# Kernel optimization log

Measured on AMD Instinct MI355X. Metric: run time of the kernel, lower is better.

Reference implementation:

```python
import jax, jax.numpy as jnp
import numpy as np

B, N, K = 8, 128, 8
N_HEADS, LATENT = 8, 128
D = N_HEADS * LATENT  # total_dim = 1024


def setup_inputs() -> dict:
    key = jax.random.key(0)
    ks = jax.random.split(key, 9)
    embedded = jax.random.normal(ks[0], (B, N, D), dtype=jnp.float32)
    # CoLight-style one-hot neighbor-selection adjacency: [B, N, K, N]
    nbr_idx = jax.random.randint(ks[1], (B, N, K), 0, N)
    adj_matrix = jax.nn.one_hot(nbr_idx, N, dtype=jnp.float32)
    s = 1.0 / np.sqrt(D)
    Wl = jax.random.uniform(ks[2], (D, D), jnp.float32, -s, s)
    bl = jax.random.uniform(ks[3], (D,), jnp.float32, -s, s)
    Wa = jax.random.uniform(ks[4], (D, D), jnp.float32, -s, s)
    ba = jax.random.uniform(ks[5], (D,), jnp.float32, -s, s)
    Wh = jax.random.uniform(ks[6], (D, D), jnp.float32, -s, s)
    bh = jax.random.uniform(ks[7], (D,), jnp.float32, -s, s)
    return {"embedded": embedded, "adj_matrix": adj_matrix,
            "Wl": Wl, "bl": bl, "Wa": Wa, "ba": ba, "Wh": Wh, "bh": bh}


def reference(embedded, adj_matrix, Wl, bl, Wa, ba, Wh, bh):
    b, n, d = embedded.shape
    H, L = N_HEADS, LATENT
    # torch: tile embedded to [B,N,N,D] then matmul with adj [B,N,K,N].
    # Equivalent without materializing the tile:
    neighbor_embed = jnp.einsum('bikn,bnd->bikd', adj_matrix, embedded)  # [B,N,K,D]

    agent = jax.nn.relu(embedded @ Wl + bl)                      # [B,N,D]
    # reshape (B,N,1,L,H) then permute (0,1,4,2,3) -> [B,N,H,1,L]
    agent_heads = agent.reshape(b, n, 1, L, H).transpose(0, 1, 4, 2, 3)

    nb = jax.nn.relu(neighbor_embed @ Wa + ba)
    neighbor_heads = nb.reshape(b, n, -1, L, H).transpose(0, 1, 4, 2, 3)  # [B,N,H,K,L]

    # einsum 'ijklm,ijknm->ijklm' with l=1: agent * sum over neighbors
    attn = agent_heads * neighbor_heads.sum(axis=3, keepdims=True)  # [B,N,H,1,L]
    attn = jax.nn.softmax(attn, axis=-1)

    nh = jax.nn.relu(neighbor_embed @ Wh + bh)
    neighbor_hidden = nh.reshape(b, n, -1, L, H).transpose(0, 1, 4, 2, 3)  # [B,N,H,K,L]

    out = attn * neighbor_hidden.sum(axis=3, keepdims=True)  # [B,N,H,1,L]
    out = out.mean(axis=2)                                   # [B,N,1,L]
    return out.reshape(b, n, -1)                             # [B,N,L]
```

## Files before the change

### kernel.cpp

```cpp
#include <hip/hip_runtime.h>
#include <math.h>

#define DD 1024
#define NN 128
#define BB 8
#define KNBR 8
#define NH 8
#define LL 128

typedef __attribute__((ext_vector_type(8))) short short8v;
typedef __attribute__((ext_vector_type(4))) float f32x4;

#define GLDS(gptr, lptr)                                                      \
  __builtin_amdgcn_global_load_lds(                                           \
      (const __attribute__((address_space(1))) void*)(gptr),                  \
      (__attribute__((address_space(3))) void*)(lptr), 16, 0, 0)

__device__ __forceinline__ unsigned short f2bf(float x) {
  unsigned u = __float_as_uint(x);
  unsigned r = u + 0x7fff + ((u >> 16) & 1);
  return (unsigned short)(r >> 16);
}
__device__ __forceinline__ float bf2f(unsigned short u) {
  return __uint_as_float((unsigned)u << 16);
}

__global__ __launch_bounds__(256)
void prep(const float* __restrict__ E,
          const float* __restrict__ Wl, const float* __restrict__ Wa,
          const float* __restrict__ Wh,
          unsigned short* __restrict__ Eb, unsigned short* __restrict__ Wt) {
  const int z = blockIdx.z;
  const int t = threadIdx.x;

  if (z == 3) {
    const int bid = blockIdx.y * 16 + blockIdx.x;
    const int i0 = bid * 4096 + t * 16;
    #pragma unroll
    for (int q = 0; q < 2; ++q) {
      const int i = i0 + q * 8;
      float4 a = *(const float4*)&E[i];
      float4 c = *(const float4*)&E[i + 4];
      union { unsigned short u[8]; uint4 v; } o;
      o.u[0] = f2bf(a.x); o.u[1] = f2bf(a.y); o.u[2] = f2bf(a.z); o.u[3] = f2bf(a.w);
      o.u[4] = f2bf(c.x); o.u[5] = f2bf(c.y); o.u[6] = f2bf(c.z); o.u[7] = f2bf(c.w);
      *(uint4*)&Eb[i] = o.v;
    }
    return;
  }

  const float* W = (z == 0) ? Wl : (z == 1) ? Wa : Wh;
  unsigned short* out = Wt + (size_t)z * DD * DD;

  __shared__ unsigned short tile[64][65];
  const int tx = t & 15, ty = t >> 4;
  const int r0 = blockIdx.y * 64, c0 = blockIdx.x * 64;

  #pragma unroll
  for (int i = 0; i < 4; ++i) {
    const int r = ty + i * 16;
    float4 v = *(const float4*)&W[(size_t)(r0 + r) * DD + c0 + tx * 4];
    tile[r][tx * 4 + 0] = f2bf(v.x);
    tile[r][tx * 4 + 1] = f2bf(v.y);
    tile[r][tx * 4 + 2] = f2bf(v.z);
    tile[r][tx * 4 + 3] = f2bf(v.w);
  }
  __syncthreads();
  #pragma unroll
  for (int i = 0; i < 4; ++i) {
    const int rr = ty + i * 16;
    ushort4 o;
    o.x = tile[tx * 4 + 0][rr];
    o.y = tile[tx * 4 + 1][rr];
    o.z = tile[tx * 4 + 2][rr];
    o.w = tile[tx * 4 + 3][rr];
    *(ushort4*)&out[(size_t)(c0 + rr) * DD + r0 + tx * 4] = o;
  }
}

__global__ __launch_bounds__(256)
void gemm3_mfma(const unsigned short* __restrict__ Eb,
                const unsigned short* __restrict__ Wt,
                const float* __restrict__ bl, const float* __restrict__ ba,
                const float* __restrict__ bh,
                float* __restrict__ Yl, unsigned short* __restrict__ Yab,
                unsigned short* __restrict__ Yhb) {
  const int orig = blockIdx.x;
  const int job = (orig & 7) * 96 + (orig >> 3);
  const int mat = job >> 8;
  const int rem = job & 255;
  const int bx = rem >> 4;
  const int by = rem & 15;

  const unsigned short* Bg = Wt + (size_t)mat * DD * DD;
  const float* bias = (mat == 0) ? bl : (mat == 1) ? ba : bh;

  __shared__ unsigned short As[3][64 * 64];
  __shared__ unsigned short Bs[3][64 * 64];

  const int t = threadIdx.x;
  const int lane = t & 63;
  const int w = t >> 6;
  const int wr = w >> 1, wc = w & 1;
  const int brow = by * 64, bcol = bx * 64;

  const int srow = t >> 3;
  const int sk = (((t & 7) ^ (srow & 7)) * 8);
  const unsigned short* gA = Eb + (size_t)(brow + srow) * DD + sk;
  const unsigned short* gB = Bg + (size_t)(bcol + srow) * DD + sk;
  const int ldsoff = w * 512;

  const int lrow = lane & 15, lg = lane >> 4;

  int aidx[2][2], bidx[2][2];
  #pragma unroll
  for (int kk = 0; kk < 2; ++kk)
    #pragma unroll
    for (int m = 0; m < 2; ++m) {
      const int ra = wr * 32 + m * 16 + lrow;
      aidx[kk][m] = ra * 64 + (((kk * 4 + lg) ^ (ra & 7)) * 8);
      const int rb = wc * 32 + m * 16 + lrow;
      bidx[kk][m] = rb * 64 + (((kk * 4 + lg) ^ (rb & 7)) * 8);
    }

  float bv0 = bias[bcol + wc * 32 + lrow];
  float bv1 = bias[bcol + wc * 32 + 16 + lrow];
  asm volatile("" : "+v"(bv0), "+v"(bv1));

  f32x4 acc[2][2] = {};

#define STAGE(q, kt) do {                                                     \
    const int k0_ = (kt) * 64;                                                \
    GLDS(gA + k0_,           &As[q][ldsoff]);                                 \
    GLDS(gA + k0_ + 32 * DD, &As[q][2048 + ldsoff]);                          \
    GLDS(gB + k0_,           &Bs[q][ldsoff]);                                 \
    GLDS(gB + k0_ + 32 * DD, &Bs[q][2048 + ldsoff]);                          \
  } while (0)

  STAGE(0, 0);
  STAGE(1, 1);

  #pragma unroll
  for (int kt = 0; kt < 16; ++kt) {
    const int p = kt % 3;
    if (kt != 15) asm volatile("s_waitcnt vmcnt(4)" ::: "memory");
    else          asm volatile("s_waitcnt vmcnt(0)" ::: "memory");
    __builtin_amdgcn_s_barrier();
    if (kt + 2 < 16) STAGE((kt + 2) % 3, kt + 2);

    short8v a[2][2], b[2][2];
    #pragma unroll
    for (int kk = 0; kk < 2; ++kk)
      #pragma unroll
      for (int m = 0; m < 2; ++m) {
        a[kk][m] = *(const short8v*)&As[p][aidx[kk][m]];
        b[kk][m] = *(const short8v*)&Bs[p][bidx[kk][m]];
      }

    #pragma unroll
    for (int kk = 0; kk < 2; ++kk)
      #pragma unroll
      for (int m = 0; m < 2; ++m)
        #pragma unroll
        for (int n = 0; n < 2; ++n)
          acc[m][n] = __builtin_amdgcn_mfma_f32_16x16x32_bf16(
              a[kk][m], b[kk][n], acc[m][n], 0, 0, 0);
  }
#undef STAGE

  #pragma unroll
  for (int m = 0; m < 2; ++m) {
    #pragma unroll
    for (int n = 0; n < 2; ++n) {
      const int col = bcol + wc * 32 + n * 16 + lrow;
      const int r0  = brow + wr * 32 + m * 16 + lg * 4;
      const float bv = n ? bv1 : bv0;
      if (mat == 0) {
        #pragma unroll
        for (int j = 0; j < 4; ++j)
          Yl[(size_t)(r0 + j) * DD + col] = fmaxf(acc[m][n][j] + bv, 0.f);
      } else {
        unsigned short* Yo = (mat == 1) ? Yab : Yhb;
        #pragma unroll
        for (int j = 0; j < 4; ++j)
          Yo[(size_t)(r0 + j) * DD + col] = f2bf(fmaxf(acc[m][n][j] + bv, 0.f));
      }
    }
  }
}

__global__ __launch_bounds__(256)
void colight_epilogue(const float* __restrict__ adj,
                      const float* __restrict__ Yl,
                      const unsigned short* __restrict__ Yab,
                      const unsigned short* __restrict__ Yhb,
                      float* __restrict__ out) {
  const int bid = blockIdx.x;
  const int bi = (bid & 7) * NN + (bid >> 3);
  const int b  = bi >> 7;

  __shared__ int   idxs[KNBR];
  __shared__ float sA[DD];
  __shared__ float sH[DD];
  __shared__ float sL[DD];
  __shared__ float sPart[NH][LL];

  const int t = threadIdx.x;

  const float* arow = adj + (size_t)bi * KNBR * NN;
  {
    const int k = t >> 5, j = t & 31;
    float4 v = *(const float4*)&arow[k * NN + j * 4];
    const int base = j * 4;
    if (v.x > 0.5f) idxs[k] = base;
    if (v.y > 0.5f) idxs[k] = base + 1;
    if (v.z > 0.5f) idxs[k] = base + 2;
    if (v.w > 0.5f) idxs[k] = base + 3;
  }
  __syncthreads();

  const int rbase = b * NN;
  int ridx[KNBR];
  #pragma unroll
  for (int k = 0; k < KNBR; ++k) ridx[k] = rbase + idxs[k];

  const int d0 = t * 4;
  {
    float a0 = 0.f, a1 = 0.f, a2 = 0.f, a3 = 0.f;
    float h0 = 0.f, h1 = 0.f, h2 = 0.f, h3 = 0.f;
    #pragma unroll
    for (int k = 0; k < KNBR; ++k) {
      const size_t rr = (size_t)ridx[k] * DD + d0;
      ushort4 va = *(const ushort4*)&Yab[rr];
      ushort4 vh = *(const ushort4*)&Yhb[rr];
      a0 += bf2f(va.x); a1 += bf2f(va.y); a2 += bf2f(va.z); a3 += bf2f(va.w);
      h0 += bf2f(vh.x); h1 += bf2f(vh.y); h2 += bf2f(vh.z); h3 += bf2f(vh.w);
    }
    float4 sa = {a0, a1, a2, a3};
    float4 sh = {h0, h1, h2, h3};
    *(float4*)&sA[d0] = sa;
    *(float4*)&sH[d0] = sh;
    *(float4*)&sL[d0] = *(const float4*)&Yl[(size_t)bi * DD + d0];
  }
  __syncthreads();

  const int h = t >> 5, j = t & 31;
  float z[4];
  float mx = -1e30f;
  #pragma unroll
  for (int q = 0; q < 4; ++q) {
    const int l = j + q * 32;
    z[q] = sL[l * NH + h] * sA[l * NH + h];
    mx = fmaxf(mx, z[q]);
  }
  #pragma unroll
  for (int m = 1; m <= 16; m <<= 1)
    mx = fmaxf(mx, __shfl_xor(mx, m, 32));

  float se = 0.f;
  #pragma unroll
  for (int q = 0; q < 4; ++q) {
    z[q] = expf(z[q] - mx);
    se += z[q];
  }
  #pragma unroll
  for (int m = 1; m <= 16; m <<= 1)
    se += __shfl_xor(se, m, 32);
  const float inv = 1.f / se;

  #pragma unroll
  for (int q = 0; q < 4; ++q) {
    const int l = j + q * 32;
    sPart[h][l] = z[q] * inv * sH[l * NH + h] * 0.125f;
  }
  __syncthreads();

  if (t < LL) {
    float o = 0.f;
    #pragma unroll
    for (int hh = 0; hh < NH; ++hh) o += sPart[hh][t];
    out[(size_t)bi * LL + t] = o;
  }
}

extern "C" void kernel_launch(void* const* d_in, const int* in_sizes, int n_in,
                              void* d_out, int out_size, void* d_ws, size_t ws_size,
                              hipStream_t stream) {
  const float* E   = (const float*)d_in[0];
  const float* adj = (const float*)d_in[1];
  const float* Wl  = (const float*)d_in[2];
  const float* bl  = (const float*)d_in[3];
  const float* Wa  = (const float*)d_in[4];
  const float* ba  = (const float*)d_in[5];
  const float* Wh  = (const float*)d_in[6];
  const float* bh  = (const float*)d_in[7];
  float* out = (float*)d_out;

  char* ws = (char*)d_ws;
  float*          Yl  = (float*)ws;
  unsigned short* Yab = (unsigned short*)(ws + 4  * 1024 * 1024);
  unsigned short* Yhb = (unsigned short*)(ws + 6  * 1024 * 1024);
  unsigned short* Eb  = (unsigned short*)(ws + 8  * 1024 * 1024);
  unsigned short* Wt  = (unsigned short*)(ws + 10 * 1024 * 1024);

  prep<<<dim3(16, 16, 4), dim3(256), 0, stream>>>(E, Wl, Wa, Wh, Eb, Wt);
  gemm3_mfma<<<dim3(768), dim3(256), 0, stream>>>(Eb, Wt, bl, ba, bh,
                                                  Yl, Yab, Yhb);
  colight_epilogue<<<dim3(BB * NN), dim3(256), 0, stream>>>(adj, Yl, Yab, Yhb, out);
}
```

Baseline: 28.89 us.

## Store agent projection in bf16, transpose epilogue LDS layout, add MFMA priority

The fp32 agent-projection output becomes bf16, so all three GEMM outputs share one store path and the epilogue reads half the bytes for that tensor. The epilogue's shared arrays are re-laid out as [head][latent], which removes the strided l*NH+h accesses that caused bank conflicts. It also wraps the MFMA loop in s_setprio and switches expf to __expf. The cost is lost precision in the agent projection and in the exponential.

```diff
diff --git a/kernel.cpp b/kernel.cpp
--- a/kernel.cpp
+++ b/kernel.cpp
@@ -83,7 +83,8 @@
                 const unsigned short* __restrict__ Wt,
                 const float* __restrict__ bl, const float* __restrict__ ba,
                 const float* __restrict__ bh,
-                float* __restrict__ Yl, unsigned short* __restrict__ Yab,
+                unsigned short* __restrict__ Ylb,
+                unsigned short* __restrict__ Yab,
                 unsigned short* __restrict__ Yhb) {
   const int orig = blockIdx.x;
   const int job = (orig & 7) * 96 + (orig >> 3);
@@ -157,6 +158,7 @@
         b[kk][m] = *(const short8v*)&Bs[p][bidx[kk][m]];
       }
 
+    __builtin_amdgcn_s_setprio(1);
     #pragma unroll
     for (int kk = 0; kk < 2; ++kk)
       #pragma unroll
@@ -165,9 +167,11 @@
         for (int n = 0; n < 2; ++n)
           acc[m][n] = __builtin_amdgcn_mfma_f32_16x16x32_bf16(
               a[kk][m], b[kk][n], acc[m][n], 0, 0, 0);
+    __builtin_amdgcn_s_setprio(0);
   }
 #undef STAGE
 
+  unsigned short* Yo = (mat == 0) ? Ylb : (mat == 1) ? Yab : Yhb;
   #pragma unroll
   for (int m = 0; m < 2; ++m) {
     #pragma unroll
@@ -175,23 +179,16 @@
       const int col = bcol + wc * 32 + n * 16 + lrow;
       const int r0  = brow + wr * 32 + m * 16 + lg * 4;
       const float bv = n ? bv1 : bv0;
-      if (mat == 0) {
-        #pragma unroll
-        for (int j = 0; j < 4; ++j)
-          Yl[(size_t)(r0 + j) * DD + col] = fmaxf(acc[m][n][j] + bv, 0.f);
-      } else {
-        unsigned short* Yo = (mat == 1) ? Yab : Yhb;
-        #pragma unroll
-        for (int j = 0; j < 4; ++j)
-          Yo[(size_t)(r0 + j) * DD + col] = f2bf(fmaxf(acc[m][n][j] + bv, 0.f));
-      }
+      #pragma unroll
+      for (int j = 0; j < 4; ++j)
+        Yo[(size_t)(r0 + j) * DD + col] = f2bf(fmaxf(acc[m][n][j] + bv, 0.f));
     }
   }
 }
 
 __global__ __launch_bounds__(256)
 void colight_epilogue(const float* __restrict__ adj,
-                      const float* __restrict__ Yl,
+                      const unsigned short* __restrict__ Ylb,
                       const unsigned short* __restrict__ Yab,
                       const unsigned short* __restrict__ Yhb,
                       float* __restrict__ out) {
@@ -200,9 +197,9 @@
   const int b  = bi >> 7;
 
   __shared__ int   idxs[KNBR];
-  __shared__ float sA[DD];
-  __shared__ float sH[DD];
-  __shared__ float sL[DD];
+  __shared__ float sA[NH][LL];
+  __shared__ float sH[NH][LL];
+  __shared__ float sL[NH][LL];
   __shared__ float sPart[NH][LL];
 
   const int t = threadIdx.x;
@@ -225,22 +222,26 @@
   for (int k = 0; k < KNBR; ++k) ridx[k] = rbase + idxs[k];
 
   const int d0 = t * 4;
+  const int gl = t >> 1;
+  const int h0 = (t & 1) * 4;
   {
     float a0 = 0.f, a1 = 0.f, a2 = 0.f, a3 = 0.f;
-    float h0 = 0.f, h1 = 0.f, h2 = 0.f, h3 = 0.f;
+    float g0 = 0.f, g1 = 0.f, g2 = 0.f, g3 = 0.f;
     #pragma unroll
     for (int k = 0; k < KNBR; ++k) {
       const size_t rr = (size_t)ridx[k] * DD + d0;
       ushort4 va = *(const ushort4*)&Yab[rr];
       ushort4 vh = *(const ushort4*)&Yhb[rr];
       a0 += bf2f(va.x); a1 += bf2f(va.y); a2 += bf2f(va.z); a3 += bf2f(va.w);
-      h0 += bf2f(vh.x); h1 += bf2f(vh.y); h2 += bf2f(vh.z); h3 += bf2f(vh.w);
+      g0 += bf2f(vh.x); g1 += bf2f(vh.y); g2 += bf2f(vh.z); g3 += bf2f(vh.w);
     }
-    float4 sa = {a0, a1, a2, a3};
-    float4 sh = {h0, h1, h2, h3};
-    *(float4*)&sA[d0] = sa;
-    *(float4*)&sH[d0] = sh;
-    *(float4*)&sL[d0] = *(const float4*)&Yl[(size_t)bi * DD + d0];
+    ushort4 vl = *(const ushort4*)&Ylb[(size_t)bi * DD + d0];
+    sA[h0 + 0][gl] = a0; sA[h0 + 1][gl] = a1;
+    sA[h0 + 2][gl] = a2; sA[h0 + 3][gl] = a3;
+    sH[h0 + 0][gl] = g0; sH[h0 + 1][gl] = g1;
+    sH[h0 + 2][gl] = g2; sH[h0 + 3][gl] = g3;
+    sL[h0 + 0][gl] = bf2f(vl.x); sL[h0 + 1][gl] = bf2f(vl.y);
+    sL[h0 + 2][gl] = bf2f(vl.z); sL[h0 + 3][gl] = bf2f(vl.w);
   }
   __syncthreads();
 
@@ -250,7 +251,7 @@
   #pragma unroll
   for (int q = 0; q < 4; ++q) {
     const int l = j + q * 32;
-    z[q] = sL[l * NH + h] * sA[l * NH + h];
+    z[q] = sL[h][l] * sA[h][l];
     mx = fmaxf(mx, z[q]);
   }
   #pragma unroll
@@ -260,7 +261,7 @@
   float se = 0.f;
   #pragma unroll
   for (int q = 0; q < 4; ++q) {
-    z[q] = expf(z[q] - mx);
+    z[q] = __expf(z[q] - mx);
     se += z[q];
   }
   #pragma unroll
@@ -271,7 +272,7 @@
   #pragma unroll
   for (int q = 0; q < 4; ++q) {
     const int l = j + q * 32;
-    sPart[h][l] = z[q] * inv * sH[l * NH + h] * 0.125f;
+    sPart[h][l] = z[q] * inv * sH[h][l] * 0.125f;
   }
   __syncthreads();
 
@@ -297,14 +298,14 @@
   float* out = (float*)d_out;
 
   char* ws = (char*)d_ws;
-  float*          Yl  = (float*)ws;
-  unsigned short* Yab = (unsigned short*)(ws + 4  * 1024 * 1024);
-  unsigned short* Yhb = (unsigned short*)(ws + 6  * 1024 * 1024);
-  unsigned short* Eb  = (unsigned short*)(ws + 8  * 1024 * 1024);
-  unsigned short* Wt  = (unsigned short*)(ws + 10 * 1024 * 1024);
+  unsigned short* Ylb = (unsigned short*)ws;
+  unsigned short* Yab = (unsigned short*)(ws + 2 * 1024 * 1024);
+  unsigned short* Yhb = (unsigned short*)(ws + 4 * 1024 * 1024);
+  unsigned short* Eb  = (unsigned short*)(ws + 6 * 1024 * 1024);
+  unsigned short* Wt  = (unsigned short*)(ws + 8 * 1024 * 1024);
 
   prep<<<dim3(16, 16, 4), dim3(256), 0, stream>>>(E, Wl, Wa, Wh, Eb, Wt);
   gemm3_mfma<<<dim3(768), dim3(256), 0, stream>>>(Eb, Wt, bl, ba, bh,
-                                                  Yl, Yab, Yhb);
-  colight_epilogue<<<dim3(BB * NN), dim3(256), 0, stream>>>(adj, Yl, Yab, Yhb, out);
-}
+                                                  Ylb, Yab, Yhb);
+  colight_epilogue<<<dim3(BB * NN), dim3(256), 0, stream>>>(adj, Ylb, Yab, Yhb, out);
+}
```

After: 27.91 us. 3.4% less time.
